# Kernel tuning notes

Measured on AMD Instinct MI355X. Metric: run time of the kernel, lower is better.

The kernel has to match this reference:

```python
import jax, jax.numpy as jnp
import numpy as np

N_NODES = 100000
D = 64


def setup_inputs() -> dict:
    key = jax.random.key(0)
    ks = jax.random.split(key, 8)
    x = jax.random.normal(ks[0], (N_NODES, D), dtype=jnp.float32)
    edge_index = jax.random.randint(ks[1], (2, 1000000), 0, N_NODES, dtype=jnp.int64)
    s = 1.0 / np.sqrt(D)
    W0 = jax.random.uniform(ks[2], (D, D), jnp.float32, -s, s)
    W1 = jax.random.uniform(ks[3], (D, D), jnp.float32, -s, s)
    W2 = jax.random.uniform(ks[4], (D, D), jnp.float32, -s, s)
    b0 = jnp.zeros((D,), jnp.float32)
    b1 = jnp.zeros((D,), jnp.float32)
    b2 = jnp.zeros((D,), jnp.float32)
    return {"x": x, "edge_index": edge_index,
            "W0": W0, "b0": b0, "W1": W1, "b1": b1, "W2": W2, "b2": b2}


def _gcn_layer(x, src, dst, norm, W, b):
    # GCNConv: h = D^{-1/2}(A+I)D^{-1/2} (x W) + b
    h = x @ W                                   # [N, D_out]
    msg = h[src] * norm[:, None]                # gather + scale, [E', D_out]
    agg = jax.ops.segment_sum(msg, dst, num_segments=x.shape[0])
    return jax.nn.relu(agg + b)


def reference(x, edge_index, W0, b0, W1, b1, W2, b2):
    n = x.shape[0]
    # add self loops (GCNConv default add_self_loops=True)
    loops = jnp.arange(n, dtype=edge_index.dtype)
    src = jnp.concatenate([edge_index[0], loops])
    dst = jnp.concatenate([edge_index[1], loops])
    # symmetric normalization deg^{-1/2}[src] * deg^{-1/2}[dst]
    deg = jax.ops.segment_sum(jnp.ones_like(src, dtype=x.dtype), dst, num_segments=n)
    dinv = jnp.where(deg > 0, jax.lax.rsqrt(deg), 0.0)
    norm = dinv[src] * dinv[dst]                # [E']
    # dropout p=0.0 / eval mode -> identity
    h = _gcn_layer(x, src, dst, norm, W0, b0)
    h = _gcn_layer(h, src, dst, norm, W1, b1)
    h = _gcn_layer(h, src, dst, norm, W2, b2)
    return h
```

## Files before the change

kernel.cpp:

```cpp
#include <hip/hip_runtime.h>
#include <hip/hip_fp16.h>

#define N_NODES 100000
#define CAP 64

typedef _Float16 v4h __attribute__((ext_vector_type(4)));
typedef float    v4f __attribute__((ext_vector_type(4)));


__global__ void k_count(const int* __restrict__ dst, int* __restrict__ deg,
                        int* __restrict__ rank, int E,
                        const float* __restrict__ W1, const float* __restrict__ W2,
                        __half* __restrict__ Wt1, __half* __restrict__ Wt2) {
    if (blockIdx.x == gridDim.x - 1) {
        for (int i = threadIdx.x; i < 4096; i += 256) {
            int k = i >> 6, c = i & 63;
            Wt1[(c << 6) + k] = __float2half(W1[i]);
            Wt2[(c << 6) + k] = __float2half(W2[i]);
        }
        return;
    }
    int i = blockIdx.x * 256 + threadIdx.x;
    int E4 = E >> 2;
    if (i < E4) {
        int4 d = ((const int4*)dst)[i];
        int4 r;
        r.x = atomicAdd(&deg[d.x], 1);
        r.y = atomicAdd(&deg[d.y], 1);
        r.z = atomicAdd(&deg[d.z], 1);
        r.w = atomicAdd(&deg[d.w], 1);
        ((int4*)rank)[i] = r;
    } else if (i == E4) {
        for (int k = E & ~3; k < E; k++)
            rank[k] = atomicAdd(&deg[dst[k]], 1);
    }
}

__global__ __launch_bounds__(256) void k_phaseB(const int* __restrict__ src,
                                                const int* __restrict__ dst,
                                                const int* __restrict__ rank,
                                                int* __restrict__ csr, int E, int FB,
                                                const float* __restrict__ in,
                                                const float* __restrict__ W,
                                                const int* __restrict__ deg,
                                                uint2* __restrict__ outh) {
    __shared__ float Ws[64 * 64];
    __shared__ float xs[16 * 65];
    if ((int)blockIdx.x < FB) {
        int i = blockIdx.x * 256 + (int)threadIdx.x;
        int E4 = E >> 2;
        if (i < E4) {
            int4 d = ((const int4*)dst)[i];
            int4 s = ((const int4*)src)[i];
            int4 r = ((const int4*)rank)[i];
            if (r.x < CAP) csr[(d.x << 6) + r.x] = s.x;
            if (r.y < CAP) csr[(d.y << 6) + r.y] = s.y;
            if (r.z < CAP) csr[(d.z << 6) + r.z] = s.z;
            if (r.w < CAP) csr[(d.w << 6) + r.w] = s.w;
        } else if (i == E4) {
            for (int k = E & ~3; k < E; k++) {
                int rr = rank[k];
                if (rr < CAP) csr[(dst[k] << 6) + rr] = src[k];
            }
        }
        return;
    }
    int bg = blockIdx.x - FB;
    int tid = threadIdx.x;

    const float4* W4 = (const float4*)W;
    float4* Ws4 = (float4*)Ws;
#pragma unroll
    for (int j = 0; j < 4; j++) Ws4[tid + j * 256] = W4[tid + j * 256];

    {
        float4 xv = ((const float4*)(in + (size_t)bg * 16 * 64))[tid];
        int f = tid * 4;
        int r = f >> 6, c = f & 63;
        xs[r * 65 + c + 0] = xv.x;
        xs[r * 65 + c + 1] = xv.y;
        xs[r * 65 + c + 2] = xv.z;
        xs[r * 65 + c + 3] = xv.w;
    }
    __syncthreads();

    int cg = tid & 15, rl = tid >> 4;
    float4 acc = {0.f, 0.f, 0.f, 0.f};
#pragma unroll
    for (int k = 0; k < 64; k++) {
        float xv = xs[rl * 65 + k];
        float4 wv = ((const float4*)Ws)[k * 16 + cg];
        acc.x += xv * wv.x;
        acc.y += xv * wv.y;
        acc.z += xv * wv.z;
        acc.w += xv * wv.w;
    }
    int row = bg * 16 + rl;
    float d = rsqrtf((float)(deg[row] + 1));
    __half2 p0 = __floats2half2_rn(acc.x * d, acc.y * d);
    __half2 p1 = __floats2half2_rn(acc.z * d, acc.w * d);
    uint2 u;
    u.x = *(unsigned int*)&p0;
    u.y = *(unsigned int*)&p1;
    outh[(size_t)row * 16 + cg] = u;
}


__device__ __forceinline__ void acc_h(float4& a, uint2 v) {
    __half2 h0 = *(__half2*)&v.x;
    __half2 h1 = *(__half2*)&v.y;
    float2 f0 = __half22float2(h0);
    float2 f1 = __half22float2(h1);
    a.x += f0.x; a.y += f0.y; a.z += f1.x; a.w += f1.y;
}

__device__ __forceinline__ float4 gather_acc(const uint2* __restrict__ h,
                                             const int* __restrict__ csr,
                                             int4 ia, int4 ib,
                                             int node, int q, int cnt) {
    const int4* c4 = (const int4*)(csr + (node << 6));
    float4 a0 = {0,0,0,0}, a1 = {0,0,0,0}, a2 = {0,0,0,0}, a3 = {0,0,0,0};
    float4 a4 = {0,0,0,0}, a5 = {0,0,0,0}, a6 = {0,0,0,0}, a7 = {0,0,0,0};
    acc_h(a0, h[(size_t)node * 16 + q]);
    int e = 0;
    for (; e + 8 <= cnt; ) {
        uint2 v0 = h[(size_t)ia.x * 16 + q];
        uint2 v1 = h[(size_t)ia.y * 16 + q];
        uint2 v2 = h[(size_t)ia.z * 16 + q];
        uint2 v3 = h[(size_t)ia.w * 16 + q];
        uint2 v4 = h[(size_t)ib.x * 16 + q];
        uint2 v5 = h[(size_t)ib.y * 16 + q];
        uint2 v6 = h[(size_t)ib.z * 16 + q];
        uint2 v7 = h[(size_t)ib.w * 16 + q];
        e += 8;
        ia = c4[e >> 2];
        ib = c4[(e >> 2) + 1];
        acc_h(a0, v0); acc_h(a1, v1); acc_h(a2, v2); acc_h(a3, v3);
        acc_h(a4, v4); acc_h(a5, v5); acc_h(a6, v6); acc_h(a7, v7);
    }
    if (e + 4 <= cnt) {
        uint2 v0 = h[(size_t)ia.x * 16 + q];
        uint2 v1 = h[(size_t)ia.y * 16 + q];
        uint2 v2 = h[(size_t)ia.z * 16 + q];
        uint2 v3 = h[(size_t)ia.w * 16 + q];
        acc_h(a4, v0); acc_h(a5, v1); acc_h(a6, v2); acc_h(a7, v3);
        e += 4;
        ia = ib;
    }
    int rem = cnt - e;
    if (rem > 0) {
        int j0 = ia.x;
        int j1 = (rem > 1) ? ia.y : j0;
        int j2 = (rem > 2) ? ia.z : j0;
        uint2 v0 = h[(size_t)j0 * 16 + q];
        uint2 v1 = h[(size_t)j1 * 16 + q];
        uint2 v2 = h[(size_t)j2 * 16 + q];
        acc_h(a1, v0);
        if (rem > 1) acc_h(a2, v1);
        if (rem > 2) acc_h(a3, v2);
    }
    float4 a;
    a.x = ((a0.x + a1.x) + (a2.x + a3.x)) + ((a4.x + a5.x) + (a6.x + a7.x));
    a.y = ((a0.y + a1.y) + (a2.y + a3.y)) + ((a4.y + a5.y) + (a6.y + a7.y));
    a.z = ((a0.z + a1.z) + (a2.z + a3.z)) + ((a4.z + a5.z) + (a6.z + a7.z));
    a.w = ((a0.w + a1.w) + (a2.w + a3.w)) + ((a4.w + a5.w) + (a6.w + a7.w));
    return a;
}

__global__ __launch_bounds__(256) void k_gather_gemm(const uint2* __restrict__ h,
                                                     const int* __restrict__ csr,
                                                     const int* __restrict__ deg,
                                                     const float* __restrict__ bias,
                                                     const __half* __restrict__ Wt,
                                                     __half* __restrict__ outh, int n) {
    __shared__ _Float16 xs_hi[16 * 68];
    __shared__ _Float16 xs_lo[16 * 68];
    __shared__ float dsv[16];
    (void)n;
    int t = threadIdx.x;
    int rl = t >> 4, q = t & 15;
    int node = blockIdx.x * 16 + rl;
    int lane = t & 63;
    int w = t >> 6;
    int col = (w << 4) + (lane & 15);
    int g = lane >> 4;

    const int4* c4 = (const int4*)(csr + (node << 6));
    int4 ia0 = c4[0];
    int4 ib0 = c4[1];
    int dg = deg[node];
    int cnt = min(dg, CAP);
    float d_i = rsqrtf((float)(dg + 1));
    if (q == 0) dsv[rl] = d_i;
    float4 b = ((const float4*)bias)[q];

    float4 a = gather_acc(h, csr, ia0, ib0, node, q, cnt);

    const v4h* wt4 = (const v4h*)(Wt + ((size_t)col << 6));
    v4h bf[4];
#pragma unroll
    for (int s = 0; s < 4; s++) bf[s] = wt4[(s << 2) + g];

    float y0 = fmaxf(fmaf(a.x, d_i, b.x), 0.f);
    float y1 = fmaxf(fmaf(a.y, d_i, b.y), 0.f);
    float y2 = fmaxf(fmaf(a.z, d_i, b.z), 0.f);
    float y3 = fmaxf(fmaf(a.w, d_i, b.w), 0.f);
    v4h yh = {(_Float16)y0, (_Float16)y1, (_Float16)y2, (_Float16)y3};
    v4h yl = {(_Float16)(y0 - (float)yh.x), (_Float16)(y1 - (float)yh.y),
              (_Float16)(y2 - (float)yh.z), (_Float16)(y3 - (float)yh.w)};
    *(v4h*)&xs_hi[rl * 68 + (q << 2)] = yh;
    *(v4h*)&xs_lo[rl * 68 + (q << 2)] = yl;
    __syncthreads();

    v4f acc = {0.f, 0.f, 0.f, 0.f};
    int arow = lane & 15;
#pragma unroll
    for (int s = 0; s < 4; s++) {
        v4h al = *(const v4h*)&xs_lo[arow * 68 + (s << 4) + (g << 2)];
        v4h ah = *(const v4h*)&xs_hi[arow * 68 + (s << 4) + (g << 2)];
        acc = __builtin_amdgcn_mfma_f32_16x16x16f16(al, bf[s], acc, 0, 0, 0);
        acc = __builtin_amdgcn_mfma_f32_16x16x16f16(ah, bf[s], acc, 0, 0, 0);
    }

#pragma unroll
    for (int j = 0; j < 4; j++) {
        int r = (g << 2) + j;
        float v = acc[j] * dsv[r];
        outh[((size_t)(blockIdx.x * 16 + r) << 6) + col] = __float2half(v);
    }
}

__global__ __launch_bounds__(256) void k_gather(const uint2* __restrict__ h,
                                                const int* __restrict__ csr,
                                                const int* __restrict__ deg,
                                                const float* __restrict__ bias,
                                                float* __restrict__ out, int n) {
    int t = threadIdx.x;
    int node = blockIdx.x * 16 + (t >> 4);
    int q = t & 15;
    if (node >= n) return;
    const int4* c4 = (const int4*)(csr + (node << 6));
    int4 ia0 = c4[0];
    int4 ib0 = c4[1];
    int dg = deg[node];
    int cnt = min(dg, CAP);
    float d = rsqrtf((float)(dg + 1));
    float4 a = gather_acc(h, csr, ia0, ib0, node, q, cnt);
    float4 b = ((const float4*)bias)[q];
    float4 r;
    r.x = fmaxf(fmaf(a.x, d, b.x), 0.f);
    r.y = fmaxf(fmaf(a.y, d, b.y), 0.f);
    r.z = fmaxf(fmaf(a.z, d, b.z), 0.f);
    r.w = fmaxf(fmaf(a.w, d, b.w), 0.f);
    ((float4*)out)[(size_t)node * 16 + q] = r;
}


extern "C" void kernel_launch(void* const* d_in, const int* in_sizes, int n_in,
                              void* d_out, int out_size, void* d_ws, size_t ws_size,
                              hipStream_t stream) {
    const float* x  = (const float*)d_in[0];
    const int*   ei = (const int*)d_in[1];
    const float* W0 = (const float*)d_in[2];
    const float* b0 = (const float*)d_in[3];
    const float* W1 = (const float*)d_in[4];
    const float* b1 = (const float*)d_in[5];
    const float* W2 = (const float*)d_in[6];
    const float* b2 = (const float*)d_in[7];
    float* out = (float*)d_out;

    const int N = N_NODES;
    int E = in_sizes[1] / 2;
    const int* src = ei;
    const int* dst = ei + E;

    char* p = (char*)d_ws;
    auto alloc = [&](size_t bytes) -> void* {
        void* r = (void*)p;
        p += (bytes + 511) & ~(size_t)511;
        return r;
    };
    int*    deg  = (int*)alloc((size_t)N * 4);
    int*    rank = (int*)alloc((size_t)E * 4 + 1024);
    int*    csr  = (int*)alloc((size_t)N * CAP * 4);
    uint2*  hA   = (uint2*)alloc((size_t)N * 64 * 2);
    uint2*  hB   = (uint2*)alloc((size_t)N * 64 * 2);
    __half* Wt1  = (__half*)alloc(4096 * 2);
    __half* Wt2  = (__half*)alloc(4096 * 2);

    const int GEMM_B = N / 16;
    const int GATH_B = (N + 15) / 16;
    const int EB = (E / 4 + 255) / 256 + 1;

    (void)hipMemsetAsync(deg, 0, (size_t)N * 4, stream);
    k_count<<<EB + 1, 256, 0, stream>>>(dst, deg, rank, E, W1, W2, Wt1, Wt2);
    k_phaseB<<<EB + GEMM_B, 256, 0, stream>>>(src, dst, rank, csr, E, EB,
                                              x, W0, deg, hA);
    k_gather_gemm<<<GATH_B, 256, 0, stream>>>(hA, csr, deg, b0, Wt1, (__half*)hB, N);
    k_gather_gemm<<<GATH_B, 256, 0, stream>>>(hB, csr, deg, b1, Wt2, (__half*)hA, N);
    k_gather<<<GATH_B, 256, 0, stream>>>(hA, csr, deg, b2, out, N);
}
```

Baseline: 250.2 us.

## Fuse degree count with CSR fill and move layer-0 GEMM to split-fp16 MFMA

Degree counting and CSR bucket filling now happen in one kernel: each edge's atomicAdd result is used directly as its slot, so the rank array and its write/read round trip are gone. Edge index loads and CSR stores use nontemporal hints. The first-layer x@W0 moves into its own kernel that uses fp16 MFMA with a hi/lo split of both operands (three MFMAs per k-step) to keep roughly fp32 accuracy. Because the GEMM now waits for the fill kernel instead of sharing a launch with it, some overlap between scatter and GEMM is lost.

```diff
diff --git a/kernel.cpp b/kernel.cpp
--- a/kernel.cpp
+++ b/kernel.cpp
@@ -6,15 +6,22 @@
 
 typedef _Float16 v4h __attribute__((ext_vector_type(4)));
 typedef float    v4f __attribute__((ext_vector_type(4)));
-
-
-__global__ void k_count(const int* __restrict__ dst, int* __restrict__ deg,
-                        int* __restrict__ rank, int E,
-                        const float* __restrict__ W1, const float* __restrict__ W2,
-                        __half* __restrict__ Wt1, __half* __restrict__ Wt2) {
+typedef int      v4i __attribute__((ext_vector_type(4)));
+
+
+__global__ void k_countfill(const int* __restrict__ src, const int* __restrict__ dst,
+                            int* __restrict__ deg, int* __restrict__ csr, int E,
+                            const float* __restrict__ W0, const float* __restrict__ W1,
+                            const float* __restrict__ W2,
+                            __half* __restrict__ Wt0h, __half* __restrict__ Wt0l,
+                            __half* __restrict__ Wt1, __half* __restrict__ Wt2) {
     if (blockIdx.x == gridDim.x - 1) {
         for (int i = threadIdx.x; i < 4096; i += 256) {
             int k = i >> 6, c = i & 63;
+            float w0 = W0[i];
+            __half w0h = __float2half(w0);
+            Wt0h[(c << 6) + k] = w0h;
+            Wt0l[(c << 6) + k] = __float2half(w0 - __half2float(w0h));
             Wt1[(c << 6) + k] = __float2half(W1[i]);
             Wt2[(c << 6) + k] = __float2half(W2[i]);
         }
@@ -23,86 +30,74 @@
     int i = blockIdx.x * 256 + threadIdx.x;
     int E4 = E >> 2;
     if (i < E4) {
-        int4 d = ((const int4*)dst)[i];
-        int4 r;
-        r.x = atomicAdd(&deg[d.x], 1);
-        r.y = atomicAdd(&deg[d.y], 1);
-        r.z = atomicAdd(&deg[d.z], 1);
-        r.w = atomicAdd(&deg[d.w], 1);
-        ((int4*)rank)[i] = r;
+        v4i d = __builtin_nontemporal_load((const v4i*)dst + i);
+        v4i s = __builtin_nontemporal_load((const v4i*)src + i);
+        int r0 = atomicAdd(&deg[d.x], 1);
+        int r1 = atomicAdd(&deg[d.y], 1);
+        int r2 = atomicAdd(&deg[d.z], 1);
+        int r3 = atomicAdd(&deg[d.w], 1);
+        if (r0 < CAP) __builtin_nontemporal_store(s.x, &csr[(d.x << 6) + r0]);
+        if (r1 < CAP) __builtin_nontemporal_store(s.y, &csr[(d.y << 6) + r1]);
+        if (r2 < CAP) __builtin_nontemporal_store(s.z, &csr[(d.z << 6) + r2]);
+        if (r3 < CAP) __builtin_nontemporal_store(s.w, &csr[(d.w << 6) + r3]);
     } else if (i == E4) {
-        for (int k = E & ~3; k < E; k++)
-            rank[k] = atomicAdd(&deg[dst[k]], 1);
-    }
-}
-
-__global__ __launch_bounds__(256) void k_phaseB(const int* __restrict__ src,
-                                                const int* __restrict__ dst,
-                                                const int* __restrict__ rank,
-                                                int* __restrict__ csr, int E, int FB,
-                                                const float* __restrict__ in,
-                                                const float* __restrict__ W,
-                                                const int* __restrict__ deg,
-                                                uint2* __restrict__ outh) {
-    __shared__ float Ws[64 * 64];
-    __shared__ float xs[16 * 65];
-    if ((int)blockIdx.x < FB) {
-        int i = blockIdx.x * 256 + (int)threadIdx.x;
-        int E4 = E >> 2;
-        if (i < E4) {
-            int4 d = ((const int4*)dst)[i];
-            int4 s = ((const int4*)src)[i];
-            int4 r = ((const int4*)rank)[i];
-            if (r.x < CAP) csr[(d.x << 6) + r.x] = s.x;
-            if (r.y < CAP) csr[(d.y << 6) + r.y] = s.y;
-            if (r.z < CAP) csr[(d.z << 6) + r.z] = s.z;
-            if (r.w < CAP) csr[(d.w << 6) + r.w] = s.w;
-        } else if (i == E4) {
-            for (int k = E & ~3; k < E; k++) {
-                int rr = rank[k];
-                if (rr < CAP) csr[(dst[k] << 6) + rr] = src[k];
-            }
+        for (int k = E & ~3; k < E; k++) {
+            int rr = atomicAdd(&deg[dst[k]], 1);
+            if (rr < CAP) csr[(dst[k] << 6) + rr] = src[k];
         }
-        return;
-    }
-    int bg = blockIdx.x - FB;
-    int tid = threadIdx.x;
-
-    const float4* W4 = (const float4*)W;
-    float4* Ws4 = (float4*)Ws;
-#pragma unroll
-    for (int j = 0; j < 4; j++) Ws4[tid + j * 256] = W4[tid + j * 256];
-
-    {
-        float4 xv = ((const float4*)(in + (size_t)bg * 16 * 64))[tid];
-        int f = tid * 4;
-        int r = f >> 6, c = f & 63;
-        xs[r * 65 + c + 0] = xv.x;
-        xs[r * 65 + c + 1] = xv.y;
-        xs[r * 65 + c + 2] = xv.z;
-        xs[r * 65 + c + 3] = xv.w;
-    }
+    }
+}
+
+__global__ __launch_bounds__(256) void k_gemm0(const float* __restrict__ x,
+                                               const __half* __restrict__ Wth,
+                                               const __half* __restrict__ Wtl,
+                                               const int* __restrict__ deg,
+                                               __half* __restrict__ outh) {
+    __shared__ _Float16 xs_hi[16 * 68];
+    __shared__ _Float16 xs_lo[16 * 68];
+    __shared__ float dsv[16];
+    int t = threadIdx.x;
+    int rl = t >> 4, q = t & 15;
+    int lane = t & 63;
+    int w = t >> 6;
+    int col = (w << 4) + (lane & 15);
+    int g = lane >> 4;
+    int node = blockIdx.x * 16 + rl;
+
+    v4f xv = __builtin_nontemporal_load((const v4f*)x + (size_t)blockIdx.x * 256 + t);
+    int dg = deg[node];
+    float d_i = rsqrtf((float)(dg + 1));
+    if (q == 0) dsv[rl] = d_i;
+
+    const v4h* wth4 = (const v4h*)(Wth + ((size_t)col << 6));
+    const v4h* wtl4 = (const v4h*)(Wtl + ((size_t)col << 6));
+    v4h bfh[4], bfl[4];
+#pragma unroll
+    for (int s = 0; s < 4; s++) { bfh[s] = wth4[(s << 2) + g]; bfl[s] = wtl4[(s << 2) + g]; }
+
+    v4h yh = {(_Float16)xv.x, (_Float16)xv.y, (_Float16)xv.z, (_Float16)xv.w};
+    v4h yl = {(_Float16)(xv.x - (float)yh.x), (_Float16)(xv.y - (float)yh.y),
+              (_Float16)(xv.z - (float)yh.z), (_Float16)(xv.w - (float)yh.w)};
+    *(v4h*)&xs_hi[rl * 68 + (q << 2)] = yh;
+    *(v4h*)&xs_lo[rl * 68 + (q << 2)] = yl;
     __syncthreads();
 
-    int cg = tid & 15, rl = tid >> 4;
-    float4 acc = {0.f, 0.f, 0.f, 0.f};
-#pragma unroll
-    for (int k = 0; k < 64; k++) {
-        float xv = xs[rl * 65 + k];
-        float4 wv = ((const float4*)Ws)[k * 16 + cg];
-        acc.x += xv * wv.x;
-        acc.y += xv * wv.y;
-        acc.z += xv * wv.z;
-        acc.w += xv * wv.w;
-    }
-    int row = bg * 16 + rl;
-    float d = rsqrtf((float)(deg[row] + 1));
-    __half2 p0 = __floats2half2_rn(acc.x * d, acc.y * d);
-    __half2 p1 = __floats2half2_rn(acc.z * d, acc.w * d);
-    uint2 u;
-    u.x = *(unsigned int*)&p0;
-    u.y = *(unsigned int*)&p1;
-    outh[(size_t)row * 16 + cg] = u;
+    v4f acc = {0.f, 0.f, 0.f, 0.f};
+    int arow = lane & 15;
+#pragma unroll
+    for (int s = 0; s < 4; s++) {
+        v4h al = *(const v4h*)&xs_lo[arow * 68 + (s << 4) + (g << 2)];
+        v4h ah = *(const v4h*)&xs_hi[arow * 68 + (s << 4) + (g << 2)];
+        acc = __builtin_amdgcn_mfma_f32_16x16x16f16(al, bfh[s], acc, 0, 0, 0);
+        acc = __builtin_amdgcn_mfma_f32_16x16x16f16(ah, bfl[s], acc, 0, 0, 0);
+        acc = __builtin_amdgcn_mfma_f32_16x16x16f16(ah, bfh[s], acc, 0, 0, 0);
+    }
+#pragma unroll
+    for (int j = 0; j < 4; j++) {
+        int r = (g << 2) + j;
+        float v = acc[j] * dsv[r];
+        outh[((size_t)(blockIdx.x * 16 + r) << 6) + col] = __float2half(v);
+    }
 }
 
 
@@ -281,10 +276,11 @@
         return r;
     };
     int*    deg  = (int*)alloc((size_t)N * 4);
-    int*    rank = (int*)alloc((size_t)E * 4 + 1024);
     int*    csr  = (int*)alloc((size_t)N * CAP * 4);
     uint2*  hA   = (uint2*)alloc((size_t)N * 64 * 2);
     uint2*  hB   = (uint2*)alloc((size_t)N * 64 * 2);
+    __half* Wt0h = (__half*)alloc(4096 * 2);
+    __half* Wt0l = (__half*)alloc(4096 * 2);
     __half* Wt1  = (__half*)alloc(4096 * 2);
     __half* Wt2  = (__half*)alloc(4096 * 2);
 
@@ -293,9 +289,9 @@
     const int EB = (E / 4 + 255) / 256 + 1;
 
     (void)hipMemsetAsync(deg, 0, (size_t)N * 4, stream);
-    k_count<<<EB + 1, 256, 0, stream>>>(dst, deg, rank, E, W1, W2, Wt1, Wt2);
-    k_phaseB<<<EB + GEMM_B, 256, 0, stream>>>(src, dst, rank, csr, E, EB,
-                                              x, W0, deg, hA);
+    k_countfill<<<EB + 1, 256, 0, stream>>>(src, dst, deg, csr, E,
+                                            W0, W1, W2, Wt0h, Wt0l, Wt1, Wt2);
+    k_gemm0<<<GEMM_B, 256, 0, stream>>>(x, Wt0h, Wt0l, deg, (__half*)hA);
     k_gather_gemm<<<GATH_B, 256, 0, stream>>>(hA, csr, deg, b0, Wt1, (__half*)hB, N);
     k_gather_gemm<<<GATH_B, 256, 0, stream>>>(hB, csr, deg, b1, Wt2, (__half*)hA, N);
     k_gather<<<GATH_B, 256, 0, stream>>>(hA, csr, deg, b2, out, N);
```

New measurement: 283.8 us. +13.4%, slower.
